# Kernel tuning notes

Hardware: AMD Instinct MI355X
Metric: run time of the kernel (lower is better)

Reference implementation:

```python
import jax, jax.numpy as jnp
import numpy as np

NUM_BINS_X = 128; NUM_BINS_Y = 128
XL, XH, YL, YH = 0.0, 1000.0, 0.0, 1000.0
NUM_NETS = 100000
NUM_NODES = 200000
NUM_MOVABLE = 180000
NUM_PINS = 400000
UNIT_H_CAP = 1.5
UNIT_V_CAP = 1.4
MAX_RATE = 2.0
MIN_RATE = 1.0 / MAX_RATE
BIN_SX = (XH - XL) / NUM_BINS_X
BIN_SY = (YH - YL) / NUM_BINS_Y


def setup_inputs() -> dict:
    key = jax.random.key(0)
    k1, k2, k3, k4, k5, k6, k7, k8 = jax.random.split(key, 8)
    pos = jnp.concatenate([
        jax.random.uniform(k1, (NUM_NODES,), jnp.float32, XL, XH - 8.0),
        jax.random.uniform(k2, (NUM_NODES,), jnp.float32, YL, YH - 8.0)])
    pin_pos = jnp.concatenate([
        jax.random.uniform(k3, (NUM_PINS,), jnp.float32, XL, XH),
        jax.random.uniform(k4, (NUM_PINS,), jnp.float32, YL, YH)])
    node_size_x = jax.random.uniform(k5, (NUM_NODES,), jnp.float32, 1.0, 8.0)
    node_size_y = jax.random.uniform(k6, (NUM_NODES,), jnp.float32, 1.0, 8.0)
    # 4 pins per net (uniform ragged layout); flat_netpin is a permutation of pins
    netpin_start = jnp.arange(NUM_NETS + 1, dtype=jnp.int32) * (NUM_PINS // NUM_NETS)
    flat_netpin = jax.random.permutation(k7, NUM_PINS).astype(jnp.int32)
    net_weights = jax.random.uniform(k8, (NUM_NETS,), jnp.float32, 0.5, 1.5)
    return dict(pos=pos, pin_pos=pin_pos, node_size_x=node_size_x,
                node_size_y=node_size_y, net_weights=net_weights,
                netpin_start=netpin_start, flat_netpin=flat_netpin)


def _bin_edges(lo, size, n):
    l = lo + jnp.arange(n, dtype=jnp.float32) * size
    return l, l + size


def _overlap(lo_e, hi_e, lo, hi):
    # per-interval overlap of [lo, hi] with each bin [lo_e, hi_e]; >=0
    return jnp.clip(jnp.minimum(hi_e[None, :], hi[:, None]) -
                    jnp.maximum(lo_e[None, :], lo[:, None]), 0.0, None)


def reference(pos, pin_pos, node_size_x, node_size_y, net_weights,
              netpin_start, flat_netpin):
    # ---- phase 1: per-net bbox (ragged gather) + RUDY demand binning ----
    lengths = netpin_start[1:] - netpin_start[:-1]                      # [N]
    net_ids = jnp.repeat(jnp.arange(NUM_NETS, dtype=jnp.int32), lengths,
                         total_repeat_length=NUM_PINS)                  # [P]
    px = pin_pos[flat_netpin]
    py = pin_pos[flat_netpin + NUM_PINS]
    x_min = jax.ops.segment_min(px, net_ids, num_segments=NUM_NETS)
    x_max = jax.ops.segment_max(px, net_ids, num_segments=NUM_NETS)
    y_min = jax.ops.segment_min(py, net_ids, num_segments=NUM_NETS)
    y_max = jax.ops.segment_max(py, net_ids, num_segments=NUM_NETS)

    bxl, bxr = _bin_edges(XL, BIN_SX, NUM_BINS_X)
    byl, byr = _bin_edges(YL, BIN_SY, NUM_BINS_Y)
    ox = _overlap(bxl, bxr, x_min, x_max)                               # [N, BX]
    oy = _overlap(byl, byr, y_min, y_max)                               # [N, BY]
    dx = x_max - x_min
    dy = y_max - y_min
    # horizontal demand per bin = wt * overlap / (y_max - y_min); vertical analog
    cx = jnp.where(dy > 0, net_weights / jnp.where(dy > 0, dy, 1.0), 0.0)
    cy = jnp.where(dx > 0, net_weights / jnp.where(dx > 0, dx, 1.0), 0.0)
    map_x = jnp.einsum('nx,ny->xy', ox * cx[:, None], oy)               # [BX, BY]
    map_y = jnp.einsum('nx,ny->xy', ox * cy[:, None], oy)

    bin_area = BIN_SX * BIN_SY
    ux = map_x / (bin_area * UNIT_H_CAP)
    uy = map_y / (bin_area * UNIT_V_CAP)
    util = jnp.clip(jnp.maximum(ux, uy), MIN_RATE, MAX_RATE)            # [BX, BY]

    # ---- phase 2: per movable node, overlap-weighted utilization read-back ----
    nx = pos[:NUM_MOVABLE]
    ny = pos[NUM_NODES:NUM_NODES + NUM_MOVABLE]
    sx = node_size_x[:NUM_MOVABLE]
    sy = node_size_y[:NUM_MOVABLE]
    oxn = _overlap(bxl, bxr, nx, nx + sx)                               # [M, BX]
    oyn = _overlap(byl, byr, ny, ny + sy)                               # [M, BY]
    tmp = jnp.einsum('mx,xy->my', oxn, util)                            # [M, BY]
    instance_route_area = jnp.sum(tmp * oyn, axis=1)                    # [M]
    return instance_route_area
```

## Files before the change

### kernel.cpp

```cpp
#include <hip/hip_runtime.h>

constexpr int   NB         = 128;
constexpr int   NCELL      = NB * NB;
constexpr int   NFL        = 2 * NCELL;
constexpr float S          = 7.8125f;
constexpr int   NUM_NETS   = 100000;
constexpr int   NUM_NODES  = 200000;
constexpr int   NUM_MOVABLE= 180000;
constexpr int   NUM_PINS   = 400000;
constexpr float UNIT_H_CAP = 1.5f;
constexpr float UNIT_V_CAP = 1.4f;

#define TPB    512
#define NDB    256
#define NCHUNK 8

__device__ __forceinline__ float edgef(int t) { return (float)t * S; }

__device__ __forceinline__ int bin_of(float v) {
    int t = (int)floorf(v / S);
    while (edgef(t + 1) <= v) ++t;
    while (edgef(t)     >  v) --t;
    return t;
}

__device__ __forceinline__ float phi(int t, float lo, float hi) {
    return fminf(fmaxf(edgef(t), lo), hi);
}

__device__ __forceinline__ int second_diff(float lo, float hi,
                                           int* idx, float* val) {
    int a = bin_of(lo);
    int b = bin_of(hi);
    int n = 0;
    idx[n] = a;
    val[n] = phi(a + 1, lo, hi) - 2.f * phi(a, lo, hi) + phi(a - 1, lo, hi);
    ++n;
    idx[n] = a + 1;
    val[n] = phi(a + 2, lo, hi) - 2.f * phi(a + 1, lo, hi) + phi(a, lo, hi);
    ++n;
    if (b > a + 1) {
        idx[n] = b;
        val[n] = phi(b + 1, lo, hi) - 2.f * phi(b, lo, hi) + phi(b - 1, lo, hi);
        ++n;
    }
    if (b > a) {
        idx[n] = b + 1;
        val[n] = phi(b + 2, lo, hi) - 2.f * phi(b + 1, lo, hi) + phi(b, lo, hi);
        ++n;
    }
    return n;
}

__global__ __launch_bounds__(TPB) void net_diff_kernel(
    const float* __restrict__ pin_pos,
    const float* __restrict__ net_weights,
    const int*   __restrict__ nps,
    const int*   __restrict__ fnp,
    float* __restrict__ P) {
    extern __shared__ float Dl[];
    const int tid = threadIdx.x;
    const int G   = gridDim.x;

    float4* D4 = (float4*)Dl;
    for (int i = tid; i < NFL / 4; i += TPB) D4[i] = make_float4(0, 0, 0, 0);
    __syncthreads();

    for (int k = tid; ; k += TPB) {
        long long nn = (long long)blockIdx.x + (long long)G * k;
        if (nn >= NUM_NETS) break;
        int n = (int)nn;
        int s = nps[n], e = nps[n + 1];
        if (e <= s) continue;
        float xmin, xmax, ymin, ymax;
        if (e - s == 4 && (s & 3) == 0) {
            int4 p4 = *(const int4*)(fnp + s);
            float x0 = pin_pos[p4.x], y0 = pin_pos[p4.x + NUM_PINS];
            float x1 = pin_pos[p4.y], y1 = pin_pos[p4.y + NUM_PINS];
            float x2 = pin_pos[p4.z], y2 = pin_pos[p4.z + NUM_PINS];
            float x3 = pin_pos[p4.w], y3 = pin_pos[p4.w + NUM_PINS];
            xmin = fminf(fminf(x0, x1), fminf(x2, x3));
            xmax = fmaxf(fmaxf(x0, x1), fmaxf(x2, x3));
            ymin = fminf(fminf(y0, y1), fminf(y2, y3));
            ymax = fmaxf(fmaxf(y0, y1), fmaxf(y2, y3));
        } else {
            xmin = 1e30f; xmax = -1e30f; ymin = 1e30f; ymax = -1e30f;
            for (int p = s; p < e; ++p) {
                int pin = fnp[p];
                float px = pin_pos[pin];
                float py = pin_pos[pin + NUM_PINS];
                xmin = fminf(xmin, px); xmax = fmaxf(xmax, px);
                ymin = fminf(ymin, py); ymax = fmaxf(ymax, py);
            }
        }
        float w  = net_weights[n];
        float dx = xmax - xmin, dy = ymax - ymin;
        float cx = (dy > 0.f) ? w / dy : 0.f;
        float cy = (dx > 0.f) ? w / dx : 0.f;
        if (cx == 0.f && cy == 0.f) continue;

        int ixs[4], iys[4];
        float vxs[4], vys[4];
        int nx = second_diff(xmin, xmax, ixs, vxs);
        int ny = second_diff(ymin, ymax, iys, vys);

        for (int i = 0; i < nx; ++i) {
            int row = ixs[i];
            float fi = vxs[i];
            if (fi == 0.f || row >= NB) continue;
            for (int j = 0; j < ny; ++j) {
                int col = iys[j];
                float t = fi * vys[j];
                if (t == 0.f || col >= NB) continue;
                int cell = row * NB + col;
                if (cx != 0.f) atomicAdd(&Dl[cell],         cx * t);
                if (cy != 0.f) atomicAdd(&Dl[NCELL + cell], cy * t);
            }
        }
    }
    __syncthreads();

    float4* Pb = (float4*)(P + (size_t)blockIdx.x * NFL);
    for (int i = tid; i < NFL / 4; i += TPB) Pb[i] = D4[i];
}

__global__ __launch_bounds__(256) void reduce_kernel(
    const float4* __restrict__ P,
    float4* __restrict__ Rc,
    int B) {
    constexpr int NF4 = NFL / 4;
    int g = blockIdx.x * blockDim.x + threadIdx.x;
    int chunk = blockIdx.y;
    int per = (B + NCHUNK - 1) / NCHUNK;
    int b0 = chunk * per;
    int b1 = min(b0 + per, B);
    float4 a0 = {0,0,0,0}, a1 = {0,0,0,0}, a2 = {0,0,0,0}, a3 = {0,0,0,0};
    int b = b0;
    for (; b + 3 < b1; b += 4) {
        float4 v0 = P[(size_t)(b    ) * NF4 + g];
        float4 v1 = P[(size_t)(b + 1) * NF4 + g];
        float4 v2 = P[(size_t)(b + 2) * NF4 + g];
        float4 v3 = P[(size_t)(b + 3) * NF4 + g];
        a0.x += v0.x; a0.y += v0.y; a0.z += v0.z; a0.w += v0.w;
        a1.x += v1.x; a1.y += v1.y; a1.z += v1.z; a1.w += v1.w;
        a2.x += v2.x; a2.y += v2.y; a2.z += v2.z; a2.w += v2.w;
        a3.x += v3.x; a3.y += v3.y; a3.z += v3.z; a3.w += v3.w;
    }
    for (; b < b1; ++b) {
        float4 v = P[(size_t)b * NF4 + g];
        a0.x += v.x; a0.y += v.y; a0.z += v.z; a0.w += v.w;
    }
    float4 r;
    r.x = (a0.x + a1.x) + (a2.x + a3.x);
    r.y = (a0.y + a1.y) + (a2.y + a3.y);
    r.z = (a0.z + a1.z) + (a2.z + a3.z);
    r.w = (a0.w + a1.w) + (a2.w + a3.w);
    Rc[(size_t)chunk * NF4 + g] = r;
}

__global__ __launch_bounds__(NB) void scan_x_kernel(
    const float* __restrict__ Rc,
    float2* __restrict__ Xp) {
    __shared__ float2 sm[NB];
    int col = blockIdx.x;
    int t = threadIdx.x;
    int idx = t * NB + col;
    float2 v = make_float2(0.f, 0.f);
    #pragma unroll
    for (int c = 0; c < NCHUNK; ++c) {
        v.x += Rc[(size_t)c * NFL + idx];
        v.y += Rc[(size_t)c * NFL + NCELL + idx];
    }
    sm[t] = v;
    __syncthreads();
    #pragma unroll
    for (int off = 1; off < NB; off <<= 1) {
        float2 cur = sm[t];
        float2 add = (t >= off) ? sm[t - off] : make_float2(0.f, 0.f);
        __syncthreads();
        cur.x += add.x; cur.y += add.y;
        sm[t] = cur;
        __syncthreads();
    }
    Xp[idx] = sm[t];
}

__global__ __launch_bounds__(NB) void scan_y_kernel(
    const float2* __restrict__ Xp,
    float* __restrict__ util) {
    __shared__ float2 sm[NB];
    int row = blockIdx.x;
    int t = threadIdx.x;
    sm[t] = Xp[row * NB + t];
    __syncthreads();
    #pragma unroll
    for (int off = 1; off < NB; off <<= 1) {
        float2 cur = sm[t];
        float2 add = (t >= off) ? sm[t - off] : make_float2(0.f, 0.f);
        __syncthreads();
        cur.x += add.x; cur.y += add.y;
        sm[t] = cur;
        __syncthreads();
    }
    constexpr float invx = 1.f / (S * S * UNIT_H_CAP);
    constexpr float invy = 1.f / (S * S * UNIT_V_CAP);
    float2 r = sm[t];
    float u = fmaxf(r.x * invx, r.y * invy);
    util[row * NB + t] = fminf(fmaxf(u, 0.5f), 2.0f);
}

__global__ __launch_bounds__(256) void node_kernel(
    const float* __restrict__ pos,
    const float* __restrict__ nsx,
    const float* __restrict__ nsy,
    const float* __restrict__ util,
    float* __restrict__ out) {
    int m = blockIdx.x * blockDim.x + threadIdx.x;
    if (m >= NUM_MOVABLE) return;
    float x  = pos[m];
    float y  = pos[NUM_NODES + m];
    float xh = x + nsx[m];
    float yh = y + nsy[m];
    int ax = max(0,      (int)floorf(x  / S) - 1);
    int bx = min(NB - 1, (int)floorf(xh / S) + 1);
    int ay = max(0,      (int)floorf(y  / S) - 1);
    int by = min(NB - 1, (int)floorf(yh / S) + 1);
    float acc = 0.f;
    for (int i = ax; i <= bx; ++i) {
        float ov = fminf(edgef(i + 1), xh) - fmaxf(edgef(i), x);
        if (ov <= 0.f) continue;
        float inner = 0.f;
        for (int j = ay; j <= by; ++j) {
            float ovy = fminf(edgef(j + 1), yh) - fmaxf(edgef(j), y);
            if (ovy > 0.f) inner += ovy * util[i * NB + j];
        }
        acc += ov * inner;
    }
    out[m] = acc;
}

extern "C" void kernel_launch(void* const* d_in, const int* in_sizes, int n_in,
                              void* d_out, int out_size, void* d_ws, size_t ws_size,
                              hipStream_t stream) {
    const float* pos      = (const float*)d_in[0];
    const float* pin_pos  = (const float*)d_in[1];
    const float* nsx      = (const float*)d_in[2];
    const float* nsy      = (const float*)d_in[3];
    const float* nw       = (const float*)d_in[4];
    const int*   npstart  = (const int*)d_in[5];
    const int*   fnp      = (const int*)d_in[6];
    float*       out      = (float*)d_out;

    float* w    = (float*)d_ws;
    float* Rc   = w;                           w += NCHUNK * NFL;
    float* Xp   = w;                           w += NFL;
    float* util = w;                           w += NCELL;
    float* P    = w;

    size_t fixed = (size_t)(w - (float*)d_ws) * sizeof(float);
    int B = NDB;
    if (ws_size > fixed) {
        size_t fit = (ws_size - fixed) / ((size_t)NFL * sizeof(float));
        if ((size_t)B > fit) B = (int)fit;
    } else {
        B = 1;
    }
    if (B < 1) B = 1;

    (void)hipFuncSetAttribute((const void*)net_diff_kernel,
                              hipFuncAttributeMaxDynamicSharedMemorySize,
                              NFL * (int)sizeof(float));

    net_diff_kernel<<<B, TPB, NFL * sizeof(float), stream>>>(
        pin_pos, nw, npstart, fnp, P);
    {
        dim3 g(NFL / 4 / 256, NCHUNK);
        reduce_kernel<<<g, 256, 0, stream>>>(
            (const float4*)P, (float4*)Rc, B);
    }
    scan_x_kernel<<<NB, NB, 0, stream>>>(Rc, (float2*)Xp);
    scan_y_kernel<<<NB, NB, 0, stream>>>((const float2*)Xp, util);
    node_kernel<<<(NUM_MOVABLE + 255) / 256, 256, 0, stream>>>(
        pos, nsx, nsy, util, out);
}
```

Before: 115.7 us.

## Replace per-block partial maps and reduce pass with global atomic accumulation

Each block now flushes its shared-memory demand map straight into one global accumulator using atomicAdd on non-zero cells, with a per-block rotation to spread contention. This removes the 256 per-block partial map writes (about 32 MB) and the separate reduce kernel that read them back. A zero kernel clears the accumulator, and nets are now given to blocks as contiguous ranges instead of strided ones. The cost is heavy global atomic traffic, since most cells are non-zero in every block, and floating-point summation order that is no longer deterministic.

```diff
diff --git a/kernel.cpp b/kernel.cpp
--- a/kernel.cpp
+++ b/kernel.cpp
@@ -13,7 +13,6 @@
 
 #define TPB    512
 #define NDB    256
-#define NCHUNK 8
 
 __device__ __forceinline__ float edgef(int t) { return (float)t * S; }
 
@@ -52,24 +51,28 @@
     return n;
 }
 
+__global__ __launch_bounds__(256) void zero_kernel(float4* __restrict__ Acc4) {
+    Acc4[blockIdx.x * 256 + threadIdx.x] = make_float4(0.f, 0.f, 0.f, 0.f);
+}
+
 __global__ __launch_bounds__(TPB) void net_diff_kernel(
     const float* __restrict__ pin_pos,
     const float* __restrict__ net_weights,
     const int*   __restrict__ nps,
     const int*   __restrict__ fnp,
-    float* __restrict__ P) {
+    float* __restrict__ Acc) {
     extern __shared__ float Dl[];
     const int tid = threadIdx.x;
-    const int G   = gridDim.x;
 
     float4* D4 = (float4*)Dl;
     for (int i = tid; i < NFL / 4; i += TPB) D4[i] = make_float4(0, 0, 0, 0);
     __syncthreads();
 
-    for (int k = tid; ; k += TPB) {
-        long long nn = (long long)blockIdx.x + (long long)G * k;
-        if (nn >= NUM_NETS) break;
-        int n = (int)nn;
+    const int per = (NUM_NETS + gridDim.x - 1) / gridDim.x;
+    const int n0  = blockIdx.x * per;
+    const int n1  = min(n0 + per, NUM_NETS);
+
+    for (int n = n0 + tid; n < n1; n += TPB) {
         int s = nps[n], e = nps[n + 1];
         if (e <= s) continue;
         float xmin, xmax, ymin, ymax;
@@ -120,57 +123,24 @@
     }
     __syncthreads();
 
-    float4* Pb = (float4*)(P + (size_t)blockIdx.x * NFL);
-    for (int i = tid; i < NFL / 4; i += TPB) Pb[i] = D4[i];
-}
-
-__global__ __launch_bounds__(256) void reduce_kernel(
-    const float4* __restrict__ P,
-    float4* __restrict__ Rc,
-    int B) {
-    constexpr int NF4 = NFL / 4;
-    int g = blockIdx.x * blockDim.x + threadIdx.x;
-    int chunk = blockIdx.y;
-    int per = (B + NCHUNK - 1) / NCHUNK;
-    int b0 = chunk * per;
-    int b1 = min(b0 + per, B);
-    float4 a0 = {0,0,0,0}, a1 = {0,0,0,0}, a2 = {0,0,0,0}, a3 = {0,0,0,0};
-    int b = b0;
-    for (; b + 3 < b1; b += 4) {
-        float4 v0 = P[(size_t)(b    ) * NF4 + g];
-        float4 v1 = P[(size_t)(b + 1) * NF4 + g];
-        float4 v2 = P[(size_t)(b + 2) * NF4 + g];
-        float4 v3 = P[(size_t)(b + 3) * NF4 + g];
-        a0.x += v0.x; a0.y += v0.y; a0.z += v0.z; a0.w += v0.w;
-        a1.x += v1.x; a1.y += v1.y; a1.z += v1.z; a1.w += v1.w;
-        a2.x += v2.x; a2.y += v2.y; a2.z += v2.z; a2.w += v2.w;
-        a3.x += v3.x; a3.y += v3.y; a3.z += v3.z; a3.w += v3.w;
-    }
-    for (; b < b1; ++b) {
-        float4 v = P[(size_t)b * NF4 + g];
-        a0.x += v.x; a0.y += v.y; a0.z += v.z; a0.w += v.w;
-    }
-    float4 r;
-    r.x = (a0.x + a1.x) + (a2.x + a3.x);
-    r.y = (a0.y + a1.y) + (a2.y + a3.y);
-    r.z = (a0.z + a1.z) + (a2.z + a3.z);
-    r.w = (a0.w + a1.w) + (a2.w + a3.w);
-    Rc[(size_t)chunk * NF4 + g] = r;
+    const int rot = (blockIdx.x << 6) & (NCELL - 1);
+    for (int i0 = tid; i0 < NCELL; i0 += TPB) {
+        int i = (i0 + rot) & (NCELL - 1);
+        float vx = Dl[i];
+        float vy = Dl[NCELL + i];
+        if (vx != 0.f) atomicAdd(&Acc[i],         vx);
+        if (vy != 0.f) atomicAdd(&Acc[NCELL + i], vy);
+    }
 }
 
 __global__ __launch_bounds__(NB) void scan_x_kernel(
-    const float* __restrict__ Rc,
+    const float* __restrict__ Acc,
     float2* __restrict__ Xp) {
     __shared__ float2 sm[NB];
     int col = blockIdx.x;
     int t = threadIdx.x;
     int idx = t * NB + col;
-    float2 v = make_float2(0.f, 0.f);
-    #pragma unroll
-    for (int c = 0; c < NCHUNK; ++c) {
-        v.x += Rc[(size_t)c * NFL + idx];
-        v.y += Rc[(size_t)c * NFL + NCELL + idx];
-    }
+    float2 v = make_float2(Acc[idx], Acc[NCELL + idx]);
     sm[t] = v;
     __syncthreads();
     #pragma unroll
@@ -252,33 +222,20 @@
     float*       out      = (float*)d_out;
 
     float* w    = (float*)d_ws;
-    float* Rc   = w;                           w += NCHUNK * NFL;
+    float* Acc  = w;                           w += NFL;
     float* Xp   = w;                           w += NFL;
     float* util = w;                           w += NCELL;
-    float* P    = w;
-
-    size_t fixed = (size_t)(w - (float*)d_ws) * sizeof(float);
-    int B = NDB;
-    if (ws_size > fixed) {
-        size_t fit = (ws_size - fixed) / ((size_t)NFL * sizeof(float));
-        if ((size_t)B > fit) B = (int)fit;
-    } else {
-        B = 1;
-    }
-    if (B < 1) B = 1;
+    (void)ws_size;
 
     (void)hipFuncSetAttribute((const void*)net_diff_kernel,
                               hipFuncAttributeMaxDynamicSharedMemorySize,
                               NFL * (int)sizeof(float));
 
-    net_diff_kernel<<<B, TPB, NFL * sizeof(float), stream>>>(
-        pin_pos, nw, npstart, fnp, P);
-    {
-        dim3 g(NFL / 4 / 256, NCHUNK);
-        reduce_kernel<<<g, 256, 0, stream>>>(
-            (const float4*)P, (float4*)Rc, B);
-    }
-    scan_x_kernel<<<NB, NB, 0, stream>>>(Rc, (float2*)Xp);
+    zero_kernel<<<NFL / 4 / 256, 256, 0, stream>>>((float4*)Acc);
+
+    net_diff_kernel<<<NDB, TPB, NFL * sizeof(float), stream>>>(
+        pin_pos, nw, npstart, fnp, Acc);
+    scan_x_kernel<<<NB, NB, 0, stream>>>(Acc, (float2*)Xp);
     scan_y_kernel<<<NB, NB, 0, stream>>>((const float2*)Xp, util);
     node_kernel<<<(NUM_MOVABLE + 255) / 256, 256, 0, stream>>>(
         pos, nsx, nsy, util, out);
```

Result: slower. 125.2 us (+8.2%).
